# Optimization experiments

Hardware: AMD Instinct MI355X
Metric: run time of the kernel (lower is better)

Reference implementation:

```python
import jax, jax.numpy as jnp
import numpy as np


def setup_inputs() -> dict:
    key = jax.random.key(0)
    k1, k2 = jax.random.split(key)
    B, H, W, D, C = 2, 128, 128, 128, 4
    image = jax.random.normal(k1, (B, H, W, D, C), dtype=jnp.float32)
    # multiplicative warp field in [0,1) keeps sample coords inside the volume
    transformation = jax.random.uniform(k2, (B, H, W, D, 3), dtype=jnp.float32)
    return {"image": image, "transformation": transformation}


def _make_grid(OH, OW, OD):
    # matches tf.meshgrid(x_lin, y_lin, z_lin) with default 'xy' indexing:
    # each output has shape (OH, OW, OD); stacked last-dim order (x, y, z)
    xl = jnp.linspace(-1.0, 1.0, OW)
    yl = jnp.linspace(-1.0, 1.0, OH)
    zl = jnp.linspace(-1.0, 1.0, OD)
    xc, yc, zc = jnp.meshgrid(xl, yl, zl, indexing="xy")
    return jnp.stack([xc, yc, zc], axis=-1)  # (OH, OW, OD, 3)


def _trilerp_one(img, coords):
    """img: (H, W, D, C); coords: (OH, OW, OD, 3) in [-1, 1]-style space."""
    H, W, D, C = img.shape
    x = 0.5 * (coords[..., 0] + 1.0) * W
    y = 0.5 * (coords[..., 1] + 1.0) * H
    z = 0.5 * (coords[..., 2] + 1.0) * D

    x0 = jnp.floor(x).astype(jnp.int32)
    y0 = jnp.floor(y).astype(jnp.int32)
    z0 = jnp.floor(z).astype(jnp.int32)
    x1 = jnp.clip(x0 + 1, 0, W - 1)
    y1 = jnp.clip(y0 + 1, 0, H - 1)
    z1 = jnp.clip(z0 + 1, 0, D - 1)
    x0 = jnp.clip(x0, 0, W - 1)
    y0 = jnp.clip(y0, 0, H - 1)
    z0 = jnp.clip(z0, 0, D - 1)

    # weights use the CLIPPED upper corners, as in the original
    dx = x1.astype(x.dtype) - x
    dy = y1.astype(y.dtype) - y
    dz = z1.astype(z.dtype) - z

    def g(yy, xx, zz):
        return img[yy, xx, zz]  # (OH, OW, OD, C) gather

    w = lambda a: a[..., None]
    out = (
        w(dz * dx * dy) * g(y0, x0, z0)
        + w(dz * dx * (1 - dy)) * g(y1, x0, z0)
        + w(dz * (1 - dx) * dy) * g(y0, x1, z0)
        + w(dz * (1 - dx) * (1 - dy)) * g(y1, x1, z0)
        + w((1 - dz) * dx * dy) * g(y0, x0, z1)
        + w((1 - dz) * dx * (1 - dy)) * g(y1, x0, z1)
        + w((1 - dz) * (1 - dx) * dy) * g(y0, x1, z1)
        + w((1 - dz) * (1 - dx) * (1 - dy)) * g(y1, x1, z1)
    )
    return out


def reference(image, transformation):
    # image: (B, H, W, D, C); transformation: (B, OH, OW, OD, 3)
    OH, OW, OD = transformation.shape[1:4]
    grid = _make_grid(OH, OW, OD)              # (OH, OW, OD, 3)
    coords = transformation * grid             # elementwise warp, as in source
    return jax.vmap(_trilerp_one, in_axes=(0, 0))(image, coords)
```

## Files before the change

kernel.cpp:

```cpp
#include <hip/hip_runtime.h>
#include <hip/hip_fp16.h>


typedef float f4 __attribute__((ext_vector_type(4)));
typedef unsigned int u32;
typedef u32 u4v __attribute__((ext_vector_type(4), aligned(8)));

__device__ inline float2 h2f(u32 b) {
    __half2 h = __builtin_bit_cast(__half2, b);
    return __half22float2(h);
}
__device__ inline u32 f2h2(float a, float b) {
    __half2 h = __floats2half2_rn(a, b);
    return __builtin_bit_cast(u32, h);
}

__global__ __launch_bounds__(256) void cvtq_kernel(
    const f4* __restrict__ img, u4v* __restrict__ rec)
{
    int t = blockIdx.x * 256 + threadIdx.x;
    int z = t & 127;
    int x = (t >> 7) & 127;
    int y = (t >> 14) & 127;
    int b = t >> 21;
    int x1 = min(x + 1, 127);
    int y1 = min(y + 1, 127);
    int bb = b << 21;

    f4 v00 = img[bb | (y  << 14) | (x  << 7) | z];
    f4 v10 = img[bb | (y1 << 14) | (x  << 7) | z];
    f4 v01 = img[bb | (y  << 14) | (x1 << 7) | z];
    f4 v11 = img[bb | (y1 << 14) | (x1 << 7) | z];

    u4v r0 = { f2h2(v00.x, v00.y), f2h2(v00.z, v00.w),
               f2h2(v10.x, v10.y), f2h2(v10.z, v10.w) };
    u4v r1 = { f2h2(v01.x, v01.y), f2h2(v01.z, v01.w),
               f2h2(v11.x, v11.y), f2h2(v11.z, v11.w) };
    __builtin_nontemporal_store(r0, rec + (size_t)t * 2);
    __builtin_nontemporal_store(r1, rec + (size_t)t * 2 + 1);
}

__global__ __launch_bounds__(256) void st3d_q_kernel(
    const u32* __restrict__ rec,
    const float* __restrict__ trans,
    f4* __restrict__ out)
{
    int bid = blockIdx.x;
    int q   = bid & 7;
    int n   = bid >> 3;
    int b   = n >> 9;
    int mA  = ((n & 511) << 8) | threadIdx.x;
    int mB  = mA + (1 << 17);

    int qi = (q >> 2) & 1;
    int qj = (q >> 1) & 1;
    int qk = q & 1;

    const float step = 2.0f / 127.0f;

#define SETUPQ(S, mval)                                                    \
    int kp##S  = (mval) & 63;                                              \
    int jp##S  = ((mval) >> 6) & 63;                                       \
    int ip##S  = (mval) >> 12;                                             \
    int ipe##S = qi ? ip##S : (63 - ip##S);                                \
    int i##S   = (qi << 6) + ipe##S;                                       \
    int j##S   = (qj << 6) + jp##S;                                        \
    int k##S   = (qk << 6) + kp##S;                                        \
    int idx##S = (((b << 7) | i##S) << 14) | (j##S << 7) | k##S;           \
    const float* t##S = trans + (size_t)idx##S * 3;                        \
    float tx##S = __builtin_nontemporal_load(t##S + 0);                    \
    float ty##S = __builtin_nontemporal_load(t##S + 1);                    \
    float tz##S = __builtin_nontemporal_load(t##S + 2);

    SETUPQ(A, mA)
    SETUPQ(B, mB)

#define GATHERQ(S)                                                         \
    float gx##S = -1.0f + step * (float)j##S;                              \
    float gy##S = -1.0f + step * (float)i##S;                              \
    float gz##S = -1.0f + step * (float)k##S;                              \
    float x##S = (tx##S * gx##S + 1.0f) * 64.0f;                           \
    float y##S = (ty##S * gy##S + 1.0f) * 64.0f;                           \
    float z##S = (tz##S * gz##S + 1.0f) * 64.0f;                           \
    int x0##S = (int)floorf(x##S);                                         \
    int y0##S = (int)floorf(y##S);                                         \
    int z0##S = (int)floorf(z##S);                                         \
    int x1##S = min(max(x0##S + 1, 0), 127);                               \
    int y1##S = min(max(y0##S + 1, 0), 127);                               \
    int z1##S = min(max(z0##S + 1, 0), 127);                               \
    x0##S = min(max(x0##S, 0), 127);                                       \
    y0##S = min(max(y0##S, 0), 127);                                       \
    z0##S = min(max(z0##S, 0), 127);                                       \
              \
    float dx##S = (float)x1##S - x##S;                                     \
    float dy##S = (float)y1##S - y##S;                                     \
    float dz##S = (float)z1##S - z##S;                                     \
    int zb##S = min(z0##S, 126);            \
    int i0##S = z0##S - zb##S;             \
    int i1##S = z1##S - zb##S;                             \
    int r##S = (((b << 7) | y0##S) << 14) | (x0##S << 7) | zb##S;          \
    const u4v* p##S = (const u4v*)(rec + (size_t)r##S * 8);                \
    u4v L0##S = p##S[0];                       \
    u4v L1##S = p##S[1];                       \
    u4v L2##S = p##S[2];                       \
    u4v L3##S = p##S[3];

    GATHERQ(A)
    GATHERQ(B)

#define ACCQ(lo0, lo1, hi0, hi1, wA, wB)                                   \
    {                                                                      \
        u32 a0 = i0s ? (hi0) : (lo0);                       \
        u32 a1 = i0s ? (hi1) : (lo1);                       \
        u32 b0 = i1s ? (hi0) : (lo0);                       \
        u32 b1 = i1s ? (hi1) : (lo1);                       \
        float2 fa0 = h2f(a0), fa1 = h2f(a1);                               \
        float2 fb0 = h2f(b0), fb1 = h2f(b1);                               \
        ox += (wA) * fa0.x + (wB) * fb0.x;                                 \
        oy += (wA) * fa0.y + (wB) * fb0.y;                                 \
        oz += (wA) * fa1.x + (wB) * fb1.x;                                 \
        ow += (wA) * fa1.y + (wB) * fb1.y;                                 \
    }

#define FINISHQ(S)                                                         \
    {                                                                      \
        float ex = 1.0f - dx##S, ey = 1.0f - dy##S, ez = 1.0f - dz##S;     \
        float wA0 = dz##S * dx##S * dy##S, wB0 = ez * dx##S * dy##S;       \
        float wA1 = dz##S * dx##S * ey,    wB1 = ez * dx##S * ey;          \
        float wA2 = dz##S * ex * dy##S,    wB2 = ez * ex * dy##S;          \
        float wA3 = dz##S * ex * ey,       wB3 = ez * ex * ey;             \
        int i0s = i0##S, i1s = i1##S;                                      \
        float ox = 0.f, oy = 0.f, oz = 0.f, ow = 0.f;                      \
        ACCQ(L0##S.x, L0##S.y, L2##S.x, L2##S.y, wA0, wB0)    \
        ACCQ(L0##S.z, L0##S.w, L2##S.z, L2##S.w, wA1, wB1)    \
        ACCQ(L1##S.x, L1##S.y, L3##S.x, L3##S.y, wA2, wB2)    \
        ACCQ(L1##S.z, L1##S.w, L3##S.z, L3##S.w, wA3, wB3)    \
        f4 o = {ox, oy, oz, ow};                                           \
        __builtin_nontemporal_store(o, &out[idx##S]);                      \
    }

    FINISHQ(A)
    FINISHQ(B)

#undef SETUPQ
#undef GATHERQ
#undef ACCQ
#undef FINISHQ
}

__global__ __launch_bounds__(256) void cvt_kernel(
    const f4* __restrict__ img, uint2* __restrict__ himg)
{
    int idx = blockIdx.x * 256 + threadIdx.x;
    f4 v = img[idx];
    __half2 lo = __floats2half2_rn(v.x, v.y);
    __half2 hi = __floats2half2_rn(v.z, v.w);
    himg[idx] = make_uint2(__builtin_bit_cast(u32, lo), __builtin_bit_cast(u32, hi));
}

__global__ __launch_bounds__(256) void st3d_h_kernel(
    const u32* __restrict__ himg,
    const float* __restrict__ trans,
    f4* __restrict__ out)
{
    int bid = blockIdx.x;
    int q   = bid & 7;
    int n   = bid >> 3;
    int b   = n >> 10;
    int m   = ((n & 1023) << 8) | threadIdx.x;

    int kp = m & 63;
    int jp = (m >> 6) & 63;
    int ip = m >> 12;

    int qi = (q >> 2) & 1;
    int qj = (q >> 1) & 1;
    int qk = q & 1;

    int ipe = qi ? ip : (63 - ip);
    int i = (qi << 6) + ipe;
    int j = (qj << 6) + jp;
    int k = (qk << 6) + kp;

    int idx = (((b << 7) | i) << 14) | (j << 7) | k;

    const float step = 2.0f / 127.0f;
    float gx = -1.0f + step * (float)j;
    float gy = -1.0f + step * (float)i;
    float gz = -1.0f + step * (float)k;

    const float* t = trans + (size_t)idx * 3;
    float tx = __builtin_nontemporal_load(t + 0);
    float ty = __builtin_nontemporal_load(t + 1);
    float tz = __builtin_nontemporal_load(t + 2);

    float x = (tx * gx + 1.0f) * 64.0f;
    float y = (ty * gy + 1.0f) * 64.0f;
    float z = (tz * gz + 1.0f) * 64.0f;

    int x0 = (int)floorf(x);
    int y0 = (int)floorf(y);
    int z0 = (int)floorf(z);
    int x1 = min(max(x0 + 1, 0), 127);
    int y1 = min(max(y0 + 1, 0), 127);
    int z1 = min(max(z0 + 1, 0), 127);
    x0 = min(max(x0, 0), 127);
    y0 = min(max(y0, 0), 127);
    z0 = min(max(z0, 0), 127);

    float dx = (float)x1 - x;
    float dy = (float)y1 - y;
    float dz = (float)z1 - z;
    float ex = 1.0f - dx;
    float ey = 1.0f - dy;
    float ez = 1.0f - dz;

    int zb = min(z0, 126);
    int i0 = z0 - zb;
    int i1 = z1 - zb;

    int bb  = b << 21;
    int ry0 = bb + (y0 << 14);
    int ry1 = bb + (y1 << 14);
    int cx0 = x0 << 7;
    int cx1 = x1 << 7;

    const u4v* p0 = (const u4v*)(himg + (size_t)(ry0 + cx0 + zb) * 2);
    const u4v* p1 = (const u4v*)(himg + (size_t)(ry1 + cx0 + zb) * 2);
    const u4v* p2 = (const u4v*)(himg + (size_t)(ry0 + cx1 + zb) * 2);
    const u4v* p3 = (const u4v*)(himg + (size_t)(ry1 + cx1 + zb) * 2);

    u4v d0 = *p0;
    u4v d1 = *p1;
    u4v d2 = *p2;
    u4v d3 = *p3;

    float wA0 = dz * dx * dy, wB0 = ez * dx * dy;
    float wA1 = dz * dx * ey, wB1 = ez * dx * ey;
    float wA2 = dz * ex * dy, wB2 = ez * ex * dy;
    float wA3 = dz * ex * ey, wB3 = ez * ex * ey;

    float ox = 0.f, oy = 0.f, oz = 0.f, ow = 0.f;

#define ACC(d, wA, wB)                                            \
    {                                                             \
        u32 a0 = i0 ? (d).z : (d).x;                              \
        u32 a1 = i0 ? (d).w : (d).y;                              \
        u32 b0 = i1 ? (d).z : (d).x;                              \
        u32 b1 = i1 ? (d).w : (d).y;                              \
        float2 fa0 = h2f(a0), fa1 = h2f(a1);                      \
        float2 fb0 = h2f(b0), fb1 = h2f(b1);                      \
        ox += (wA) * fa0.x + (wB) * fb0.x;                        \
        oy += (wA) * fa0.y + (wB) * fb0.y;                        \
        oz += (wA) * fa1.x + (wB) * fb1.x;                        \
        ow += (wA) * fa1.y + (wB) * fb1.y;                        \
    }

    ACC(d0, wA0, wB0)
    ACC(d1, wA1, wB1)
    ACC(d2, wA2, wB2)
    ACC(d3, wA3, wB3)
#undef ACC

    f4 o = {ox, oy, oz, ow};
    __builtin_nontemporal_store(o, &out[idx]);
}

__global__ __launch_bounds__(256) void st3d_kernel(
    const float* __restrict__ img,
    const float* __restrict__ trans,
    f4* __restrict__ out)
{
    int bid = blockIdx.x;
    int q   = bid & 7;
    int n   = bid >> 3;
    int b   = n >> 10;
    int m   = ((n & 1023) << 8) | threadIdx.x;

    int kp = m & 63;
    int jp = (m >> 6) & 63;
    int ip = m >> 12;

    int qi = (q >> 2) & 1;
    int qj = (q >> 1) & 1;
    int qk = q & 1;

    int ipe = qi ? ip : (63 - ip);
    int i = (qi << 6) + ipe;
    int j = (qj << 6) + jp;
    int k = (qk << 6) + kp;

    int idx = (((b << 7) | i) << 14) | (j << 7) | k;

    const float step = 2.0f / 127.0f;
    float gx = -1.0f + step * (float)j;
    float gy = -1.0f + step * (float)i;
    float gz = -1.0f + step * (float)k;

    const float* t = trans + (size_t)idx * 3;
    float tx = __builtin_nontemporal_load(t + 0);
    float ty = __builtin_nontemporal_load(t + 1);
    float tz = __builtin_nontemporal_load(t + 2);

    float x = (tx * gx + 1.0f) * 64.0f;
    float y = (ty * gy + 1.0f) * 64.0f;
    float z = (tz * gz + 1.0f) * 64.0f;

    int x0 = (int)floorf(x);
    int y0 = (int)floorf(y);
    int z0 = (int)floorf(z);
    int x1 = min(max(x0 + 1, 0), 127);
    int y1 = min(max(y0 + 1, 0), 127);
    int z1 = min(max(z0 + 1, 0), 127);
    x0 = min(max(x0, 0), 127);
    y0 = min(max(y0, 0), 127);
    z0 = min(max(z0, 0), 127);

    float dx = (float)x1 - x;
    float dy = (float)y1 - y;
    float dz = (float)z1 - z;
    float ex = 1.0f - dx;
    float ey = 1.0f - dy;
    float ez = 1.0f - dz;

    const f4* img4 = (const f4*)img;
    int bb  = b << 21;
    int ry0 = bb + (y0 << 14);
    int ry1 = bb + (y1 << 14);
    int cx0 = x0 << 7;
    int cx1 = x1 << 7;

    int A0 = ry0 + cx0 + z0;
    int A1 = ry1 + cx0 + z0;
    int A2 = ry0 + cx1 + z0;
    int A3 = ry1 + cx1 + z0;
    int dzi = z1 - z0;

    f4 c000 = img4[A0];
    f4 c100 = img4[A1];
    f4 c010 = img4[A2];
    f4 c110 = img4[A3];
    f4 c001 = img4[A0 + dzi];
    f4 c101 = img4[A1 + dzi];
    f4 c011 = img4[A2 + dzi];
    f4 c111 = img4[A3 + dzi];

    float w000 = dz * dx * dy;
    float w100 = dz * dx * ey;
    float w010 = dz * ex * dy;
    float w110 = dz * ex * ey;
    float w001 = ez * dx * dy;
    float w101 = ez * dx * ey;
    float w011 = ez * ex * dy;
    float w111 = ez * ex * ey;

    f4 o = w000*c000 + w100*c100 + w010*c010 + w110*c110
         + w001*c001 + w101*c101 + w011*c011 + w111*c111;

    __builtin_nontemporal_store(o, &out[idx]);
}

extern "C" void kernel_launch(void* const* d_in, const int* in_sizes, int n_in,
                              void* d_out, int out_size, void* d_ws, size_t ws_size,
                              hipStream_t stream) {
    const float* img   = (const float*)d_in[0];
    const float* trans = (const float*)d_in[1];
    f4* out = (f4*)d_out;

    int N = in_sizes[1] / 3;
    int block = 256;

    size_t need_q = (size_t)N * 32;
    size_t need_h = (size_t)N * 8;

    if (ws_size >= need_q) {
        cvtq_kernel<<<N / block, block, 0, stream>>>((const f4*)img, (u4v*)d_ws);
        st3d_q_kernel<<<N / (2 * block), block, 0, stream>>>(
            (const u32*)d_ws, trans, out);
    } else if (ws_size >= need_h) {
        cvt_kernel<<<N / block, block, 0, stream>>>((const f4*)img, (uint2*)d_ws);
        st3d_h_kernel<<<N / block, block, 0, stream>>>(
            (const u32*)d_ws, trans, out);
    } else {
        st3d_kernel<<<N / block, block, 0, stream>>>(img, trans, out);
    }
}
```

Before: 229.8 us.

## Split convert and sample kernels per batch to keep workspace cache-resident

Launches the fp16 neighbor-record conversion and the trilinear sampling kernel once per batch instead of once over both batches, so each batch's 64MB record table is produced and then consumed while still in the large last-level cache. The conversion stores become normal stores instead of nontemporal, so the records stay cached for the following sample kernel. This adds two extra launches and smaller grids per launch, and the batch stride is hardcoded to 2^21.

```diff
diff --git a/kernel.cpp b/kernel.cpp
--- a/kernel.cpp
+++ b/kernel.cpp
@@ -16,40 +16,40 @@
 }
 
 __global__ __launch_bounds__(256) void cvtq_kernel(
-    const f4* __restrict__ img, u4v* __restrict__ rec)
+    const f4* __restrict__ img, u4v* __restrict__ rec, int bb)
 {
     int t = blockIdx.x * 256 + threadIdx.x;
     int z = t & 127;
     int x = (t >> 7) & 127;
-    int y = (t >> 14) & 127;
-    int b = t >> 21;
+    int y = t >> 14;
     int x1 = min(x + 1, 127);
     int y1 = min(y + 1, 127);
-    int bb = b << 21;
 
     f4 v00 = img[bb | (y  << 14) | (x  << 7) | z];
     f4 v10 = img[bb | (y1 << 14) | (x  << 7) | z];
     f4 v01 = img[bb | (y  << 14) | (x1 << 7) | z];
     f4 v11 = img[bb | (y1 << 14) | (x1 << 7) | z];
 
+    int tt = bb | t;
+
     u4v r0 = { f2h2(v00.x, v00.y), f2h2(v00.z, v00.w),
                f2h2(v10.x, v10.y), f2h2(v10.z, v10.w) };
     u4v r1 = { f2h2(v01.x, v01.y), f2h2(v01.z, v01.w),
                f2h2(v11.x, v11.y), f2h2(v11.z, v11.w) };
-    __builtin_nontemporal_store(r0, rec + (size_t)t * 2);
-    __builtin_nontemporal_store(r1, rec + (size_t)t * 2 + 1);
+    rec[(size_t)tt * 2]     = r0;
+    rec[(size_t)tt * 2 + 1] = r1;
 }
 
 __global__ __launch_bounds__(256) void st3d_q_kernel(
     const u32* __restrict__ rec,
     const float* __restrict__ trans,
-    f4* __restrict__ out)
+    f4* __restrict__ out,
+    int bb)
 {
     int bid = blockIdx.x;
     int q   = bid & 7;
     int n   = bid >> 3;
-    int b   = n >> 9;
-    int mA  = ((n & 511) << 8) | threadIdx.x;
+    int mA  = (n << 8) | threadIdx.x;
     int mB  = mA + (1 << 17);
 
     int qi = (q >> 2) & 1;
@@ -62,11 +62,11 @@
     int kp##S  = (mval) & 63;                                              \
     int jp##S  = ((mval) >> 6) & 63;                                       \
     int ip##S  = (mval) >> 12;                                             \
-    int ipe##S = qi ? ip##S : (63 - ip##S);                                \
+    int ipe##S = qi ? ip##S : (63 - ip##S);      \
     int i##S   = (qi << 6) + ipe##S;                                       \
     int j##S   = (qj << 6) + jp##S;                                        \
     int k##S   = (qk << 6) + kp##S;                                        \
-    int idx##S = (((b << 7) | i##S) << 14) | (j##S << 7) | k##S;           \
+    int idx##S = bb | (i##S << 14) | (j##S << 7) | k##S;                   \
     const float* t##S = trans + (size_t)idx##S * 3;                        \
     float tx##S = __builtin_nontemporal_load(t##S + 0);                    \
     float ty##S = __builtin_nontemporal_load(t##S + 1);                    \
@@ -98,7 +98,7 @@
     int zb##S = min(z0##S, 126);            \
     int i0##S = z0##S - zb##S;             \
     int i1##S = z1##S - zb##S;                             \
-    int r##S = (((b << 7) | y0##S) << 14) | (x0##S << 7) | zb##S;          \
+    int r##S = bb | (y0##S << 14) | (x0##S << 7) | zb##S;                  \
     const u4v* p##S = (const u4v*)(rec + (size_t)r##S * 8);                \
     u4v L0##S = p##S[0];                       \
     u4v L1##S = p##S[1];                       \
@@ -368,15 +368,20 @@
     f4* out = (f4*)d_out;
 
     int N = in_sizes[1] / 3;
+    int NB = 1 << 21;
     int block = 256;
 
     size_t need_q = (size_t)N * 32;
     size_t need_h = (size_t)N * 8;
 
     if (ws_size >= need_q) {
-        cvtq_kernel<<<N / block, block, 0, stream>>>((const f4*)img, (u4v*)d_ws);
-        st3d_q_kernel<<<N / (2 * block), block, 0, stream>>>(
-            (const u32*)d_ws, trans, out);
+        for (int b = 0; b < 2; ++b) {
+            int bb = b << 21;
+            cvtq_kernel<<<NB / block, block, 0, stream>>>(
+                (const f4*)img, (u4v*)d_ws, bb);
+            st3d_q_kernel<<<NB / (2 * block), block, 0, stream>>>(
+                (const u32*)d_ws, trans, out, bb);
+        }
     } else if (ws_size >= need_h) {
         cvt_kernel<<<N / block, block, 0, stream>>>((const f4*)img, (uint2*)d_ws);
         st3d_h_kernel<<<N / block, block, 0, stream>>>(
```

Measured after the change: 227.9 us. No clear change (-0.8%).
